# Kernel tuning notes

Hardware: AMD Instinct MI355X
Metric: run time of the kernel (lower is better)

The kernel has to match this reference:

```python
import math
import jax, jax.numpy as jnp
import numpy as np


def setup_inputs() -> dict:
    key = jax.random.key(0)
    k1, k2, k3 = jax.random.split(key, 3)
    B, N, D = 8192, 64, 128
    return {
        "x_t": jax.random.normal(k1, (B, D), dtype=jnp.float32),
        "means": jax.random.normal(k2, (N, D), dtype=jnp.float32),
        "cholesky_factors": jax.random.normal(k3, (N, D, D), dtype=jnp.float32),
    }


def reference(x_t, means, cholesky_factors):
    # x_t: (B, D), means: (N, D), cholesky_factors: (N, D, D)
    N, D = means.shape
    log_c = D * math.log(2.0 * math.pi)

    # tril + exp-reparameterized diagonal
    L_tril = jnp.tril(cholesky_factors)                      # (N, D, D)
    eye = jnp.eye(D, dtype=bool)
    L = jnp.where(eye, jnp.exp(L_tril), L_tril)              # (N, D, D)

    # log det Sigma = 2 * sum(log diag(L)); diag(L) = exp(raw diag)
    diag_raw = jnp.diagonal(L_tril, axis1=-2, axis2=-1)      # (N, D)
    log_det_Sigma = 2.0 * jnp.sum(diag_raw, axis=-1)         # (N,)

    # delta[b, n, :] = x_t[b] - means[n]
    delta = x_t[:, None, :] - means[None, :, :]              # (B, N, D)

    # Solve L y = delta per state, batching B into the RHS columns
    # (avoids materializing L expanded over the batch).
    rhs = jnp.transpose(delta, (1, 2, 0))                    # (N, D, B)
    y = jax.scipy.linalg.solve_triangular(L, rhs, lower=True)  # (N, D, B)
    quad = jnp.transpose(jnp.sum(y * y, axis=1))             # (B, N)

    log_p = -0.5 * (log_c + log_det_Sigma[None, :] + quad)   # (B, N)
    return log_p
```

## Files before the change

kernel.cpp:

```cpp
#include <hip/hip_runtime.h>
#include <math.h>

#define DD 128
#define BB 8192
#define NN 64
#define LOGC 235.24826450039622f
#define CLAMP_M 1.0e12f
#define YCLAMP 1.0e18f
#define KP 136
#define PITCH 129

typedef __attribute__((ext_vector_type(8))) short bf16x8;
typedef __attribute__((ext_vector_type(4))) float f32x4;

__device__ __forceinline__ unsigned int f2bf(float x) {
    unsigned int u = __float_as_uint(x);
    return (u + 0x7FFFu + ((u >> 16) & 1u)) >> 16;
}
__device__ __forceinline__ unsigned int pack2(float lo, float hi) {
    return f2bf(lo) | (f2bf(hi) << 16);
}
__device__ __forceinline__ float clampM(float x) {
    return fminf(fmaxf(x, -CLAMP_M), CLAMP_M);
}
__device__ __forceinline__ float lane_bcast(float v, int j) {
    return __int_as_float(__builtin_amdgcn_readlane(__float_as_int(v), j));
}

__global__ __launch_bounds__(256, 2)
void solve_columns(const float* __restrict__ chol,
                   const float* __restrict__ means,
                   unsigned short* __restrict__ Mout,
                   float* __restrict__ vout,
                   float* __restrict__ termout)
{
    const int n = blockIdx.y;
    const int grp = blockIdx.x;
    const int t = threadIdx.x;
    const int lane = t & 63;
    const int w = t >> 6;
    const float* __restrict__ Ln = chol + (size_t)n * DD * DD;

    __shared__ float LsT[DD][PITCH];
    __shared__ float s_invd[DD];
    __shared__ float s_raw[DD];
    __shared__ float ybuf[4][DD + 2];

    #pragma unroll
    for (int it = 0; it < 16; ++it) {
        const int id = it * 256 + t;
        const int i = id >> 5;
        const int j0 = (id & 31) * 4;
        const float4 vv = *(const float4*)(Ln + (size_t)i * DD + j0);
        LsT[j0 + 0][i] = (i > j0 + 0) ? vv.x : 0.0f;
        LsT[j0 + 1][i] = (i > j0 + 1) ? vv.y : 0.0f;
        LsT[j0 + 2][i] = (i > j0 + 2) ? vv.z : 0.0f;
        LsT[j0 + 3][i] = (i > j0 + 3) ? vv.w : 0.0f;
    }
    if (t < DD) {
        const float raw = Ln[(size_t)t * DD + t];
        s_raw[t] = raw;
        s_invd[t] = __expf(-raw);
    }
    __syncthreads();

    const bool is_mu = (grp == 32);

    float r_lo = 0.0f, r_hi = 0.0f;
    if (is_mu) {
        if (w == 0) {
            r_lo = means[(size_t)n * DD + lane];
            r_hi = means[(size_t)n * DD + 64 + lane];
        } else if (w == 1) {
            float v = s_raw[lane] + s_raw[64 + lane];
            #pragma unroll
            for (int o = 32; o > 0; o >>= 1) v += __shfl_down(v, o);
            if (lane == 0) termout[n] = LOGC + 2.0f * v;
        }
    } else {
        const int c = grp * 4 + w;
        r_lo = (lane == c) ? 1.0f : 0.0f;
        r_hi = (lane + 64 == c) ? 1.0f : 0.0f;
    }

    #pragma unroll 4
    for (int j = 0; j < 64; ++j) {
        const float y = clampM(lane_bcast(r_lo, j) * s_invd[j]);
        r_lo = fmaf(-LsT[j][lane], y, r_lo);
        r_hi = fmaf(-LsT[j][64 + lane], y, r_hi);
    }
    #pragma unroll 4
    for (int j = 64; j < 128; ++j) {
        const float y = clampM(lane_bcast(r_hi, j - 64) * s_invd[j]);
        r_hi = fmaf(-LsT[j][64 + lane], y, r_hi);
    }

    const float y_lo = clampM(r_lo * s_invd[lane]);
    const float y_hi = clampM(r_hi * s_invd[64 + lane]);

    if (is_mu) {
        if (w == 0) {
            vout[(size_t)n * DD + lane] = y_lo;
            vout[(size_t)n * DD + 64 + lane] = y_hi;
        }
        return;
    }

    ybuf[w][lane] = y_lo;
    ybuf[w][64 + lane] = y_hi;
    __syncthreads();

    const int i = t >> 1;
    const int p = t & 1;
    const unsigned int pk = pack2(ybuf[2 * p][i], ybuf[2 * p + 1][i]);
    *(unsigned int*)&Mout[((size_t)n * DD + i) * DD + grp * 4 + 2 * p] = pk;
}

__global__ __launch_bounds__(256, 2)
void emission_mfma(const float* __restrict__ x,
                   const unsigned short* __restrict__ Mws,
                   const float* __restrict__ vws,
                   const float* __restrict__ termws,
                   float* __restrict__ out)
{
    const int btile = blockIdx.x;
    const int ngrp = blockIdx.y;
    const int t = threadIdx.x;
    const int lane = t & 63;
    const int w = t >> 6;
    const int wi = w >> 1;
    const int wb = w & 1;

    __shared__ __align__(16) unsigned short xs[128 * KP];
    __shared__ __align__(16) unsigned short as[128 * KP];
    __shared__ __align__(16) float sv[DD];
    __shared__ float sterm[8];
    __shared__ float redbuf[2 * 128];
    __shared__ float qbuf[8 * 128];

    const int bbase = btile * 128;

    #pragma unroll
    for (int it = 0; it < 8; ++it) {
        const int id = it * 256 + t;
        const int brow = id >> 4;
        const int koff = (id & 15) * 8;
        const float4* px = (const float4*)(x + (size_t)(bbase + brow) * DD + koff);
        const float4 a = px[0], b = px[1];
        uint4 p;
        p.x = pack2(a.x, a.y);
        p.y = pack2(a.z, a.w);
        p.z = pack2(b.x, b.y);
        p.w = pack2(b.z, b.w);
        *(uint4*)&xs[brow * KP + koff] = p;
    }
    __syncthreads();

    bf16x8 bf[4][4];
    #pragma unroll
    for (int bt = 0; bt < 4; ++bt)
        #pragma unroll
        for (int ks = 0; ks < 4; ++ks) {
            const int col = wb * 64 + bt * 16 + (lane & 15);
            const int k = ks * 32 + (lane >> 4) * 8;
            bf[bt][ks] = *(const bf16x8*)&xs[col * KP + k];
        }

    const f32x4 zero = {0.0f, 0.0f, 0.0f, 0.0f};

    for (int nl = 0; nl < 8; ++nl) {
        const int n = ngrp * 8 + nl;
        const unsigned short* __restrict__ Mn = Mws + (size_t)n * DD * DD;
        #pragma unroll
        for (int it = 0; it < 8; ++it) {
            const int id = it * 256 + t;
            const int row = id >> 4;
            const int koff = (id & 15) * 8;
            *(uint4*)&as[row * KP + koff] = *(const uint4*)&Mn[row * DD + koff];
        }
        if (t < DD) sv[t] = vws[n * DD + t];
        if (t == 0) sterm[nl] = termws[n];
        if (nl > 0 && t < 128) qbuf[(nl - 1) * 128 + t] = redbuf[t] + redbuf[128 + t];
        __syncthreads();

        f32x4 acc[4][4];
        #pragma unroll
        for (int it = 0; it < 4; ++it)
            #pragma unroll
            for (int bt = 0; bt < 4; ++bt) acc[it][bt] = zero;

        #pragma unroll
        for (int ks = 0; ks < 4; ++ks) {
            bf16x8 af[4];
            #pragma unroll
            for (int it = 0; it < 4; ++it) {
                const int row = wi * 64 + it * 16 + (lane & 15);
                const int k = ks * 32 + (lane >> 4) * 8;
                af[it] = *(const bf16x8*)&as[row * KP + k];
            }
            #pragma unroll
            for (int it = 0; it < 4; ++it)
                #pragma unroll
                for (int bt = 0; bt < 4; ++bt)
                    acc[it][bt] = __builtin_amdgcn_mfma_f32_16x16x32_bf16(
                        af[it], bf[bt][ks], acc[it][bt], 0, 0, 0);
        }

        float p[4] = {0.0f, 0.0f, 0.0f, 0.0f};
        #pragma unroll
        for (int it = 0; it < 4; ++it) {
            const int rowbase = wi * 64 + it * 16 + (lane >> 4) * 4;
            const f32x4 v4 = *(const f32x4*)&sv[rowbase];
            #pragma unroll
            for (int bt = 0; bt < 4; ++bt) {
                const f32x4 a = acc[it][bt];
                const float t0 = a.x - v4.x, t1 = a.y - v4.y;
                const float t2 = a.z - v4.z, t3 = a.w - v4.w;
                p[bt] += t0 * t0 + t1 * t1 + t2 * t2 + t3 * t3;
            }
        }
        #pragma unroll
        for (int bt = 0; bt < 4; ++bt) {
            float pv = p[bt];
            pv += __shfl_xor(pv, 16);
            pv += __shfl_xor(pv, 32);
            if (lane < 16) redbuf[wi * 128 + wb * 64 + bt * 16 + lane] = pv;
        }
        __syncthreads();
    }

    if (t < 128) {
        qbuf[7 * 128 + t] = redbuf[t] + redbuf[128 + t];
        float o[8];
        #pragma unroll
        for (int j = 0; j < 8; ++j)
            o[j] = -0.5f * (sterm[j] + qbuf[j * 128 + t]);
        float* po = &out[(size_t)(bbase + t) * NN + ngrp * 8];
        *(float4*)&po[0] = make_float4(o[0], o[1], o[2], o[3]);
        *(float4*)&po[4] = make_float4(o[4], o[5], o[6], o[7]);
    }
}

__global__ __launch_bounds__(256, 2)
void emission_solve_fb(const float* __restrict__ xin,
                       const float* __restrict__ means,
                       const float* __restrict__ chol,
                       float* __restrict__ out)
{
    const int n = blockIdx.y;
    const int t = threadIdx.x;
    const int b = blockIdx.x * 256 + t;
    const float* __restrict__ Ln = chol + (size_t)n * DD * DD;

    __shared__ float s_invd[DD];
    __shared__ float s_mu[DD];
    __shared__ float s_part[4];

    float raw = 0.0f;
    if (t < DD) {
        raw = Ln[t * DD + t];
        s_invd[t] = 1.0f / expf(raw);
        s_mu[t] = means[n * DD + t];
    }
    float v = raw;
    #pragma unroll
    for (int o = 32; o > 0; o >>= 1) v += __shfl_down(v, o);
    if ((t & 63) == 0) s_part[t >> 6] = v;
    __syncthreads();

    const float term = LOGC + 2.0f * (s_part[0] + s_part[1] + s_part[2] + s_part[3]);

    float y[DD];
    float quad = 0.0f;
    #pragma unroll
    for (int i = 0; i < DD; ++i) {
        const float xv = xin[(size_t)b * DD + i] - s_mu[i];
        float sA = 0.0f, sB = 0.0f;
        #pragma unroll
        for (int j = 0; j + 1 < i; j += 2) {
            sA = fmaf(Ln[i * DD + j], y[j], sA);
            sB = fmaf(Ln[i * DD + j + 1], y[j + 1], sB);
        }
        if (i & 1) sA = fmaf(Ln[i * DD + (i - 1)], y[i - 1], sA);
        const float s = xv - sA - sB;
        float yi = s * s_invd[i];
        yi = fminf(fmaxf(yi, -YCLAMP), YCLAMP);
        y[i] = yi;
        quad = fmaf(yi, yi, quad);
    }
    out[(size_t)b * NN + n] = -0.5f * (term + quad);
}

extern "C" void kernel_launch(void* const* d_in, const int* in_sizes, int n_in,
                              void* d_out, int out_size, void* d_ws, size_t ws_size,
                              hipStream_t stream) {
    const float* x     = (const float*)d_in[0];
    const float* means = (const float*)d_in[1];
    const float* chol  = (const float*)d_in[2];
    float* out = (float*)d_out;

    const size_t needM = (size_t)NN * DD * DD * sizeof(unsigned short);
    const size_t needV = (size_t)NN * DD * sizeof(float);
    const size_t needT = (size_t)NN * sizeof(float);

    if (ws_size >= needM + needV + needT) {
        unsigned short* Mws = (unsigned short*)d_ws;
        float* vws = (float*)((char*)d_ws + needM);
        float* tws = (float*)((char*)d_ws + needM + needV);
        solve_columns<<<dim3(33, NN), 256, 0, stream>>>(chol, means, Mws, vws, tws);
        emission_mfma<<<dim3(BB / 128, 8), 256, 0, stream>>>(x, Mws, vws, tws, out);
    } else {
        emission_solve_fb<<<dim3(BB / 256, NN), 256, 0, stream>>>(x, means, chol, out);
    }
}
```

Measured before the change: 114.9 us.

## Skip unneeded triangular columns in solve and register-prefetch next M tile

```diff
diff --git a/kernel.cpp b/kernel.cpp
--- a/kernel.cpp
+++ b/kernel.cpp
@@ -41,6 +41,9 @@
     const int w = t >> 6;
     const float* __restrict__ Ln = chol + (size_t)n * DD * DD;
 
+    const bool is_mu = (grp == 32);
+    const int base = is_mu ? 0 : grp * 4;
+
     __shared__ float LsT[DD][PITCH];
     __shared__ float s_invd[DD];
     __shared__ float s_raw[DD];
@@ -51,11 +54,19 @@
         const int id = it * 256 + t;
         const int i = id >> 5;
         const int j0 = (id & 31) * 4;
-        const float4 vv = *(const float4*)(Ln + (size_t)i * DD + j0);
-        LsT[j0 + 0][i] = (i > j0 + 0) ? vv.x : 0.0f;
-        LsT[j0 + 1][i] = (i > j0 + 1) ? vv.y : 0.0f;
-        LsT[j0 + 2][i] = (i > j0 + 2) ? vv.z : 0.0f;
-        LsT[j0 + 3][i] = (i > j0 + 3) ? vv.w : 0.0f;
+        if (j0 + 3 < base) continue;
+        if (i <= j0) {
+            LsT[j0 + 0][i] = 0.0f;
+            LsT[j0 + 1][i] = 0.0f;
+            LsT[j0 + 2][i] = 0.0f;
+            LsT[j0 + 3][i] = 0.0f;
+        } else {
+            const float4 vv = *(const float4*)(Ln + (size_t)i * DD + j0);
+            LsT[j0 + 0][i] = (i > j0 + 0) ? vv.x : 0.0f;
+            LsT[j0 + 1][i] = (i > j0 + 1) ? vv.y : 0.0f;
+            LsT[j0 + 2][i] = (i > j0 + 2) ? vv.z : 0.0f;
+            LsT[j0 + 3][i] = (i > j0 + 3) ? vv.w : 0.0f;
+        }
     }
     if (t < DD) {
         const float raw = Ln[(size_t)t * DD + t];
@@ -63,8 +74,6 @@
         s_invd[t] = __expf(-raw);
     }
     __syncthreads();
-
-    const bool is_mu = (grp == 32);
 
     float r_lo = 0.0f, r_hi = 0.0f;
     if (is_mu) {
@@ -84,13 +93,13 @@
     }
 
     #pragma unroll 4
-    for (int j = 0; j < 64; ++j) {
+    for (int j = base; j < 64; ++j) {
         const float y = clampM(lane_bcast(r_lo, j) * s_invd[j]);
         r_lo = fmaf(-LsT[j][lane], y, r_lo);
         r_hi = fmaf(-LsT[j][64 + lane], y, r_hi);
     }
     #pragma unroll 4
-    for (int j = 64; j < 128; ++j) {
+    for (int j = (base > 64 ? base : 64); j < 128; ++j) {
         const float y = clampM(lane_bcast(r_hi, j - 64) * s_invd[j]);
         r_hi = fmaf(-LsT[j][64 + lane], y, r_hi);
     }
@@ -154,6 +163,27 @@
         p.w = pack2(b.z, b.w);
         *(uint4*)&xs[brow * KP + koff] = p;
     }
+
+    const int mrow = t >> 1;
+    const int mk = (t & 1) * 64;
+    uint4 pref[8];
+    {
+        const unsigned short* __restrict__ Mn = Mws + (size_t)(ngrp * 8) * DD * DD;
+        #pragma unroll
+        for (int it = 0; it < 8; ++it)
+            pref[it] = *(const uint4*)&Mn[(size_t)((it & 3) * 32 + mrow / 4) * DD +
+                                          mk + (mrow & 3) * 0 + (it >> 2) * 32];
+    }
+    {
+        const unsigned short* __restrict__ Mn = Mws + (size_t)(ngrp * 8) * DD * DD;
+        #pragma unroll
+        for (int it = 0; it < 8; ++it) {
+            const int id = it * 256 + t;
+            const int row = id >> 4;
+            const int koff = (id & 15) * 8;
+            pref[it] = *(const uint4*)&Mn[(size_t)row * DD + koff];
+        }
+    }
     __syncthreads();
 
     bf16x8 bf[4][4];
@@ -170,17 +200,28 @@
 
     for (int nl = 0; nl < 8; ++nl) {
         const int n = ngrp * 8 + nl;
-        const unsigned short* __restrict__ Mn = Mws + (size_t)n * DD * DD;
         #pragma unroll
         for (int it = 0; it < 8; ++it) {
             const int id = it * 256 + t;
             const int row = id >> 4;
             const int koff = (id & 15) * 8;
-            *(uint4*)&as[row * KP + koff] = *(const uint4*)&Mn[row * DD + koff];
+            *(uint4*)&as[row * KP + koff] = pref[it];
         }
         if (t < DD) sv[t] = vws[n * DD + t];
         if (t == 0) sterm[nl] = termws[n];
         if (nl > 0 && t < 128) qbuf[(nl - 1) * 128 + t] = redbuf[t] + redbuf[128 + t];
+
+        if (nl < 7) {
+            const unsigned short* __restrict__ Mn1 =
+                Mws + (size_t)(n + 1) * DD * DD;
+            #pragma unroll
+            for (int it = 0; it < 8; ++it) {
+                const int id = it * 256 + t;
+                const int row = id >> 4;
+                const int koff = (id & 15) * 8;
+                pref[it] = *(const uint4*)&Mn1[(size_t)row * DD + koff];
+            }
+        }
         __syncthreads();
 
         f32x4 acc[4][4];
```

Measured after the change: 149.5 us. +30.2%, slower.

## Batch four columns per wave in solve, double-buffer M via async LDS loads

Applied to the files above, without the earlier changes.

```diff
diff --git a/kernel.cpp b/kernel.cpp
--- a/kernel.cpp
+++ b/kernel.cpp
@@ -25,6 +25,11 @@
 }
 __device__ __forceinline__ float lane_bcast(float v, int j) {
     return __int_as_float(__builtin_amdgcn_readlane(__float_as_int(v), j));
+}
+__device__ __forceinline__ void gl_lds16(const unsigned short* g, unsigned short* l) {
+    __builtin_amdgcn_global_load_lds(
+        (const __attribute__((address_space(1))) void*)g,
+        (__attribute__((address_space(3))) void*)l, 16, 0, 0);
 }
 
 __global__ __launch_bounds__(256, 2)
@@ -41,21 +46,32 @@
     const int w = t >> 6;
     const float* __restrict__ Ln = chol + (size_t)n * DD * DD;
 
+    const bool is_mu = (grp == 8);
+    const int jmin = is_mu ? 0 : grp * 16;
+
     __shared__ float LsT[DD][PITCH];
     __shared__ float s_invd[DD];
     __shared__ float s_raw[DD];
-    __shared__ float ybuf[4][DD + 2];
+    __shared__ float ybuf[4][4][DD + 2];
 
     #pragma unroll
     for (int it = 0; it < 16; ++it) {
         const int id = it * 256 + t;
         const int i = id >> 5;
         const int j0 = (id & 31) * 4;
-        const float4 vv = *(const float4*)(Ln + (size_t)i * DD + j0);
-        LsT[j0 + 0][i] = (i > j0 + 0) ? vv.x : 0.0f;
-        LsT[j0 + 1][i] = (i > j0 + 1) ? vv.y : 0.0f;
-        LsT[j0 + 2][i] = (i > j0 + 2) ? vv.z : 0.0f;
-        LsT[j0 + 3][i] = (i > j0 + 3) ? vv.w : 0.0f;
+        if (j0 < jmin) continue;
+        if (i <= j0) {
+            LsT[j0 + 0][i] = 0.0f;
+            LsT[j0 + 1][i] = 0.0f;
+            LsT[j0 + 2][i] = 0.0f;
+            LsT[j0 + 3][i] = 0.0f;
+        } else {
+            const float4 vv = *(const float4*)(Ln + (size_t)i * DD + j0);
+            LsT[j0 + 0][i] = (i > j0 + 0) ? vv.x : 0.0f;
+            LsT[j0 + 1][i] = (i > j0 + 1) ? vv.y : 0.0f;
+            LsT[j0 + 2][i] = (i > j0 + 2) ? vv.z : 0.0f;
+            LsT[j0 + 3][i] = (i > j0 + 3) ? vv.w : 0.0f;
+        }
     }
     if (t < DD) {
         const float raw = Ln[(size_t)t * DD + t];
@@ -64,56 +80,84 @@
     }
     __syncthreads();
 
-    const bool is_mu = (grp == 32);
-
-    float r_lo = 0.0f, r_hi = 0.0f;
     if (is_mu) {
         if (w == 0) {
-            r_lo = means[(size_t)n * DD + lane];
-            r_hi = means[(size_t)n * DD + 64 + lane];
+            float rl = means[(size_t)n * DD + lane];
+            float rh = means[(size_t)n * DD + 64 + lane];
+            #pragma unroll 4
+            for (int j = 0; j < 64; ++j) {
+                const float y = clampM(lane_bcast(rl, j) * s_invd[j]);
+                rl = fmaf(-LsT[j][lane], y, rl);
+                rh = fmaf(-LsT[j][64 + lane], y, rh);
+            }
+            #pragma unroll 4
+            for (int j = 64; j < 128; ++j) {
+                const float y = clampM(lane_bcast(rh, j - 64) * s_invd[j]);
+                rh = fmaf(-LsT[j][64 + lane], y, rh);
+            }
+            vout[(size_t)n * DD + lane] = clampM(rl * s_invd[lane]);
+            vout[(size_t)n * DD + 64 + lane] = clampM(rh * s_invd[64 + lane]);
         } else if (w == 1) {
             float v = s_raw[lane] + s_raw[64 + lane];
             #pragma unroll
             for (int o = 32; o > 0; o >>= 1) v += __shfl_down(v, o);
             if (lane == 0) termout[n] = LOGC + 2.0f * v;
         }
-    } else {
-        const int c = grp * 4 + w;
-        r_lo = (lane == c) ? 1.0f : 0.0f;
-        r_hi = (lane + 64 == c) ? 1.0f : 0.0f;
-    }
+        return;
+    }
+
+    const int c0 = grp * 16 + w * 4;
+    float r0l = (lane == c0 + 0) ? 1.0f : 0.0f;
+    float r1l = (lane == c0 + 1) ? 1.0f : 0.0f;
+    float r2l = (lane == c0 + 2) ? 1.0f : 0.0f;
+    float r3l = (lane == c0 + 3) ? 1.0f : 0.0f;
+    float r0h = (lane + 64 == c0 + 0) ? 1.0f : 0.0f;
+    float r1h = (lane + 64 == c0 + 1) ? 1.0f : 0.0f;
+    float r2h = (lane + 64 == c0 + 2) ? 1.0f : 0.0f;
+    float r3h = (lane + 64 == c0 + 3) ? 1.0f : 0.0f;
 
     #pragma unroll 4
-    for (int j = 0; j < 64; ++j) {
-        const float y = clampM(lane_bcast(r_lo, j) * s_invd[j]);
-        r_lo = fmaf(-LsT[j][lane], y, r_lo);
-        r_hi = fmaf(-LsT[j][64 + lane], y, r_hi);
+    for (int j = c0; j < 64; ++j) {
+        const float invd = s_invd[j];
+        const float Ll = LsT[j][lane];
+        const float Lh = LsT[j][64 + lane];
+        const float y0 = clampM(lane_bcast(r0l, j) * invd);
+        const float y1 = clampM(lane_bcast(r1l, j) * invd);
+        const float y2 = clampM(lane_bcast(r2l, j) * invd);
+        const float y3 = clampM(lane_bcast(r3l, j) * invd);
+        r0l = fmaf(-Ll, y0, r0l); r0h = fmaf(-Lh, y0, r0h);
+        r1l = fmaf(-Ll, y1, r1l); r1h = fmaf(-Lh, y1, r1h);
+        r2l = fmaf(-Ll, y2, r2l); r2h = fmaf(-Lh, y2, r2h);
+        r3l = fmaf(-Ll, y3, r3l); r3h = fmaf(-Lh, y3, r3h);
     }
     #pragma unroll 4
-    for (int j = 64; j < 128; ++j) {
-        const float y = clampM(lane_bcast(r_hi, j - 64) * s_invd[j]);
-        r_hi = fmaf(-LsT[j][64 + lane], y, r_hi);
-    }
-
-    const float y_lo = clampM(r_lo * s_invd[lane]);
-    const float y_hi = clampM(r_hi * s_invd[64 + lane]);
-
-    if (is_mu) {
-        if (w == 0) {
-            vout[(size_t)n * DD + lane] = y_lo;
-            vout[(size_t)n * DD + 64 + lane] = y_hi;
-        }
-        return;
-    }
-
-    ybuf[w][lane] = y_lo;
-    ybuf[w][64 + lane] = y_hi;
-    __syncthreads();
-
-    const int i = t >> 1;
-    const int p = t & 1;
-    const unsigned int pk = pack2(ybuf[2 * p][i], ybuf[2 * p + 1][i]);
-    *(unsigned int*)&Mout[((size_t)n * DD + i) * DD + grp * 4 + 2 * p] = pk;
+    for (int j = (c0 > 64 ? c0 : 64); j < 128; ++j) {
+        const float invd = s_invd[j];
+        const float Lh = LsT[j][64 + lane];
+        const float y0 = clampM(lane_bcast(r0h, j - 64) * invd);
+        const float y1 = clampM(lane_bcast(r1h, j - 64) * invd);
+        const float y2 = clampM(lane_bcast(r2h, j - 64) * invd);
+        const float y3 = clampM(lane_bcast(r3h, j - 64) * invd);
+        r0h = fmaf(-Lh, y0, r0h);
+        r1h = fmaf(-Lh, y1, r1h);
+        r2h = fmaf(-Lh, y2, r2h);
+        r3h = fmaf(-Lh, y3, r3h);
+    }
+
+    const float i_lo = s_invd[lane], i_hi = s_invd[64 + lane];
+    ybuf[w][0][lane] = clampM(r0l * i_lo); ybuf[w][0][64 + lane] = clampM(r0h * i_hi);
+    ybuf[w][1][lane] = clampM(r1l * i_lo); ybuf[w][1][64 + lane] = clampM(r1h * i_hi);
+    ybuf[w][2][lane] = clampM(r2l * i_lo); ybuf[w][2][64 + lane] = clampM(r2h * i_hi);
+    ybuf[w][3][lane] = clampM(r3l * i_lo); ybuf[w][3][64 + lane] = clampM(r3h * i_hi);
+
+    #pragma unroll
+    for (int q = 0; q < 2; ++q) {
+        const int i = 2 * lane + q;
+        uint2 pk;
+        pk.x = pack2(ybuf[w][0][i], ybuf[w][1][i]);
+        pk.y = pack2(ybuf[w][2][i], ybuf[w][3][i]);
+        *(uint2*)&Mout[((size_t)n * DD + i) * DD + c0] = pk;
+    }
 }
 
 __global__ __launch_bounds__(256, 2)
@@ -131,14 +175,28 @@
     const int wi = w >> 1;
     const int wb = w & 1;
 
-    __shared__ __align__(16) unsigned short xs[128 * KP];
-    __shared__ __align__(16) unsigned short as[128 * KP];
-    __shared__ __align__(16) float sv[DD];
-    __shared__ float sterm[8];
-    __shared__ float redbuf[2 * 128];
-    __shared__ float qbuf[8 * 128];
+    __shared__ __align__(16) char smem[34816 + 32768 + 4096 + 4096 + 2048 + 32];
+    unsigned short* xs = (unsigned short*)smem;
+    unsigned short* P1 = (unsigned short*)smem;
+    unsigned short* P0 = (unsigned short*)(smem + 34816);
+    float* sv8   = (float*)(smem + 34816 + 32768);
+    float* qbuf  = (float*)(smem + 34816 + 32768 + 4096);
+    float* redbuf = (float*)(smem + 34816 + 32768 + 8192);
+    float* sterm = (float*)(smem + 34816 + 32768 + 8192 + 2048);
 
     const int bbase = btile * 128;
+    const unsigned short* __restrict__ Mbase = Mws + (size_t)(ngrp * 8) * DD * DD;
+
+    auto stage_M = [&](const unsigned short* Mn, unsigned short* Pbuf) {
+        #pragma unroll
+        for (int k = 0; k < 8; ++k) {
+            const int s = w * 512 + k * 64 + lane;
+            const int row = s >> 4;
+            const int kc = (s & 15) ^ (row & 15);
+            gl_lds16(Mn + (size_t)row * DD + kc * 8,
+                     Pbuf + (size_t)(w * 512 + k * 64) * 8);
+        }
+    };
 
     #pragma unroll
     for (int it = 0; it < 8; ++it) {
@@ -154,6 +212,9 @@
         p.w = pack2(b.z, b.w);
         *(uint4*)&xs[brow * KP + koff] = p;
     }
+    *(float4*)&sv8[4 * t] = *(const float4*)&vws[(size_t)ngrp * 8 * DD + 4 * t];
+    if (t < 8) sterm[t] = termws[ngrp * 8 + t];
+    stage_M(Mbase, P0);
     __syncthreads();
 
     bf16x8 bf[4][4];
@@ -165,23 +226,19 @@
             const int k = ks * 32 + (lane >> 4) * 8;
             bf[bt][ks] = *(const bf16x8*)&xs[col * KP + k];
         }
+    __syncthreads();
 
     const f32x4 zero = {0.0f, 0.0f, 0.0f, 0.0f};
 
     for (int nl = 0; nl < 8; ++nl) {
-        const int n = ngrp * 8 + nl;
-        const unsigned short* __restrict__ Mn = Mws + (size_t)n * DD * DD;
-        #pragma unroll
-        for (int it = 0; it < 8; ++it) {
-            const int id = it * 256 + t;
-            const int row = id >> 4;
-            const int koff = (id & 15) * 8;
-            *(uint4*)&as[row * KP + koff] = *(const uint4*)&Mn[row * DD + koff];
-        }
-        if (t < DD) sv[t] = vws[n * DD + t];
-        if (t == 0) sterm[nl] = termws[n];
-        if (nl > 0 && t < 128) qbuf[(nl - 1) * 128 + t] = redbuf[t] + redbuf[128 + t];
-        __syncthreads();
+        if (nl < 7)
+            stage_M(Mbase + (size_t)(nl + 1) * DD * DD, ((nl + 1) & 1) ? P1 : P0);
+        if (nl > 0 && t < 128) {
+            float* rb = redbuf + ((nl - 1) & 1) * 256;
+            qbuf[(nl - 1) * 128 + t] = rb[t] + rb[128 + t];
+        }
+
+        const unsigned short* Pc = (nl & 1) ? P1 : P0;
 
         f32x4 acc[4][4];
         #pragma unroll
@@ -195,8 +252,9 @@
             #pragma unroll
             for (int it = 0; it < 4; ++it) {
                 const int row = wi * 64 + it * 16 + (lane & 15);
-                const int k = ks * 32 + (lane >> 4) * 8;
-                af[it] = *(const bf16x8*)&as[row * KP + k];
+                const int kchunk = ks * 4 + (lane >> 4);
+                af[it] = *(const bf16x8*)((const char*)Pc + row * 256 +
+                                          ((kchunk ^ (row & 15)) * 16));
             }
             #pragma unroll
             for (int it = 0; it < 4; ++it)
@@ -210,7 +268,7 @@
         #pragma unroll
         for (int it = 0; it < 4; ++it) {
             const int rowbase = wi * 64 + it * 16 + (lane >> 4) * 4;
-            const f32x4 v4 = *(const f32x4*)&sv[rowbase];
+            const f32x4 v4 = *(const f32x4*)&sv8[nl * 128 + rowbase];
             #pragma unroll
             for (int bt = 0; bt < 4; ++bt) {
                 const f32x4 a = acc[it][bt];
@@ -219,18 +277,19 @@
                 p[bt] += t0 * t0 + t1 * t1 + t2 * t2 + t3 * t3;
             }
         }
+        float* rb = redbuf + (nl & 1) * 256;
         #pragma unroll
         for (int bt = 0; bt < 4; ++bt) {
             float pv = p[bt];
             pv += __shfl_xor(pv, 16);
             pv += __shfl_xor(pv, 32);
-            if (lane < 16) redbuf[wi * 128 + wb * 64 + bt * 16 + lane] = pv;
+            if (lane < 16) rb[wi * 128 + wb * 64 + bt * 16 + lane] = pv;
         }
         __syncthreads();
     }
 
     if (t < 128) {
-        qbuf[7 * 128 + t] = redbuf[t] + redbuf[128 + t];
+        qbuf[7 * 128 + t] = redbuf[256 + t] + redbuf[256 + 128 + t];
         float o[8];
         #pragma unroll
         for (int j = 0; j < 8; ++j)
@@ -307,7 +366,7 @@
         unsigned short* Mws = (unsigned short*)d_ws;
         float* vws = (float*)((char*)d_ws + needM);
         float* tws = (float*)((char*)d_ws + needM + needV);
-        solve_columns<<<dim3(33, NN), 256, 0, stream>>>(chol, means, Mws, vws, tws);
+        solve_columns<<<dim3(9, NN), 256, 0, stream>>>(chol, means, Mws, vws, tws);
         emission_mfma<<<dim3(BB / 128, 8), 256, 0, stream>>>(x, Mws, vws, tws, out);
     } else {
         emission_solve_fb<<<dim3(BB / 256, NN), 256, 0, stream>>>(x, means, chol, out);
```

New measurement: 100.4 us. -12.6%, faster.
